# Performance work log

Hardware: AMD Instinct MI355X
Metric: run time of the kernel (lower is better)

Reference implementation:

```python
import jax, jax.numpy as jnp
import numpy as np

ENC_DIM = 1024
NUM_HEADS = 16
HEAD_DIM = ENC_DIM // NUM_HEADS
D_FF = 4 * ENC_DIM
EPS = 1e-5


def _layernorm(x, g, b):
    mu = jnp.mean(x, axis=-1, keepdims=True)
    var = jnp.mean((x - mu) ** 2, axis=-1, keepdims=True)
    return (x - mu) * jax.lax.rsqrt(var + EPS) * g + b


def setup_inputs() -> dict:
    key = jax.random.key(0)
    ks = jax.random.split(key, 12)
    s = 1.0 / np.sqrt(ENC_DIM)
    sf = 1.0 / np.sqrt(D_FF)
    x = jax.random.normal(ks[0], (2, 2048, ENC_DIM), dtype=jnp.float32)
    return {
        "x": x,
        "ln1_g": jnp.ones((ENC_DIM,), jnp.float32),
        "ln1_b": jnp.zeros((ENC_DIM,), jnp.float32),
        "wq": jax.random.uniform(ks[1], (ENC_DIM, ENC_DIM), jnp.float32, -s, s),
        "bq": jax.random.uniform(ks[2], (ENC_DIM,), jnp.float32, -s, s),
        "wk": jax.random.uniform(ks[3], (ENC_DIM, ENC_DIM), jnp.float32, -s, s),
        "bk": jax.random.uniform(ks[4], (ENC_DIM,), jnp.float32, -s, s),
        "wv": jax.random.uniform(ks[5], (ENC_DIM, ENC_DIM), jnp.float32, -s, s),
        "bv": jax.random.uniform(ks[6], (ENC_DIM,), jnp.float32, -s, s),
        "wo": jax.random.uniform(ks[7], (ENC_DIM, ENC_DIM), jnp.float32, -s, s),
        "bo": jax.random.uniform(ks[8], (ENC_DIM,), jnp.float32, -s, s),
        "w1": jax.random.uniform(ks[9], (ENC_DIM, D_FF), jnp.float32, -s, s),
        "b1": jax.random.uniform(ks[10], (D_FF,), jnp.float32, -s, s),
        "w2": jax.random.uniform(ks[11], (D_FF, ENC_DIM), jnp.float32, -sf, sf),
        "b2": jnp.zeros((ENC_DIM,), jnp.float32),
        "ln2_g": jnp.ones((ENC_DIM,), jnp.float32),
        "ln2_b": jnp.zeros((ENC_DIM,), jnp.float32),
    }


def reference(x, ln1_g, ln1_b, wq, bq, wk, bk, wv, bv, wo, bo, w1, b1, w2, b2, ln2_g, ln2_b):
    B, S, D = x.shape
    h = _layernorm(x, ln1_g, ln1_b)
    # QKV projections -> (B, H, S, hd)
    def split_heads(t):
        return t.reshape(B, S, NUM_HEADS, HEAD_DIM).transpose(0, 2, 1, 3)
    q = split_heads(h @ wq + bq)
    k = split_heads(h @ wk + bk)
    v = split_heads(h @ wv + bv)
    scores = jnp.einsum("bhqd,bhkd->bhqk", q, k) / np.sqrt(HEAD_DIM)
    probs = jax.nn.softmax(scores, axis=-1)
    attn = jnp.einsum("bhqk,bhkd->bhqd", probs, v)
    attn = attn.transpose(0, 2, 1, 3).reshape(B, S, D)
    x = attn @ wo + bo + x  # residual 1
    h2 = _layernorm(x, ln2_g, ln2_b)
    mlp = jax.nn.gelu(h2 @ w1 + b1, approximate=False) @ w2 + b2
    return x + mlp
```

## Files before the change

kernel.cpp:

```cpp
#include <hip/hip_runtime.h>

typedef unsigned short u16;
typedef unsigned int u32;
typedef __bf16 bf16x8 __attribute__((ext_vector_type(8)));
typedef float floatx4 __attribute__((ext_vector_type(4)));

__device__ __forceinline__ u16 f2bf(float f) {
    u32 u = __float_as_uint(f);
    u = (u + 0x7FFFu + ((u >> 16) & 1u)) >> 16;
    return (u16)u;
}

__device__ __forceinline__ void gld_lds16(const u16* g, u16* l) {
    __builtin_amdgcn_global_load_lds(
        (const __attribute__((address_space(1))) u32*)g,
        (__attribute__((address_space(3))) u32*)l, 16, 0, 0);
}

__device__ __forceinline__ float gelu_exact(float v) {
    const float z = fabsf(v) * 0.70710678118f;
    const float t = __builtin_amdgcn_rcpf(1.0f + 0.3275911f * z);
    const float e = __builtin_amdgcn_exp2f(-z * z * 1.44269504f);
    float poly = 1.061405429f;
    poly = poly * t - 1.453152027f;
    poly = poly * t + 1.421413741f;
    poly = poly * t - 0.284496736f;
    poly = poly * t + 0.254829592f;
    float erfz = 1.0f - poly * t * e;
    erfz = copysignf(erfz, v);
    return 0.5f * v * (1.0f + erfz);
}

__global__ __launch_bounds__(256) void transpose_cvt4(
    const float* __restrict__ s0, const float* __restrict__ s1,
    const float* __restrict__ s2, const float* __restrict__ s3,
    u16* __restrict__ d0, u16* __restrict__ d1,
    u16* __restrict__ d2, u16* __restrict__ d3)
{
    __shared__ float t[32][33];
    const int z = blockIdx.z;
    const float* src = z == 0 ? s0 : (z == 1 ? s1 : (z == 2 ? s2 : s3));
    u16* dst = z == 0 ? d0 : (z == 1 ? d1 : (z == 2 ? d2 : d3));
    const int bm = blockIdx.x * 32, bk = blockIdx.y * 32;
    const int tx = threadIdx.x & 31, ty = threadIdx.x >> 5;
    #pragma unroll
    for (int i = ty; i < 32; i += 8)
        t[i][tx] = src[(long)(bk + i) * 1024 + bm + tx];
    __syncthreads();
    #pragma unroll
    for (int i = ty; i < 32; i += 8)
        dst[(long)(bm + i) * 1024 + bk + tx] = f2bf(t[tx][i]);
}

__global__ __launch_bounds__(256) void transpose_cvt(
    const float* __restrict__ src, u16* __restrict__ dst, int K, int M)
{
    __shared__ float t[32][33];
    const int bm = blockIdx.x * 32, bk = blockIdx.y * 32;
    const int tx = threadIdx.x & 31, ty = threadIdx.x >> 5;
    #pragma unroll
    for (int i = ty; i < 32; i += 8)
        t[i][tx] = src[(long)(bk + i) * M + bm + tx];
    __syncthreads();
    #pragma unroll
    for (int i = ty; i < 32; i += 8)
        dst[(long)(bm + i) * K + bk + tx] = f2bf(t[tx][i]);
}

__global__ __launch_bounds__(256) void ln_kernel(
    const float* __restrict__ x, const float* __restrict__ g,
    const float* __restrict__ bta, u16* __restrict__ out)
{
    const int row = blockIdx.x;
    const int tid = threadIdx.x;
    const float4 v = ((const float4*)(x + (long)row * 1024))[tid];
    float s  = v.x + v.y + v.z + v.w;
    float s2 = v.x*v.x + v.y*v.y + v.z*v.z + v.w*v.w;
    #pragma unroll
    for (int off = 1; off < 64; off <<= 1) {
        s  += __shfl_xor(s, off);
        s2 += __shfl_xor(s2, off);
    }
    __shared__ float red[8];
    const int wave = tid >> 6, lane = tid & 63;
    if (lane == 0) { red[wave] = s; red[4 + wave] = s2; }
    __syncthreads();
    s  = red[0] + red[1] + red[2] + red[3];
    s2 = red[4] + red[5] + red[6] + red[7];
    const float mu   = s * (1.0f / 1024.0f);
    const float var  = s2 * (1.0f / 1024.0f) - mu * mu;
    const float rstd = rsqrtf(var + 1e-5f);
    const int c = tid << 2;
    ushort4 o;
    o.x = f2bf((v.x - mu) * rstd * g[c + 0] + bta[c + 0]);
    o.y = f2bf((v.y - mu) * rstd * g[c + 1] + bta[c + 1]);
    o.z = f2bf((v.z - mu) * rstd * g[c + 2] + bta[c + 2]);
    o.w = f2bf((v.w - mu) * rstd * g[c + 3] + bta[c + 3]);
    ((ushort4*)(out + (long)row * 1024))[tid] = o;
}

__global__ __launch_bounds__(256) void add_kernel(
    float* __restrict__ out, const float* __restrict__ p1)
{
    const int t = blockIdx.x * 256 + threadIdx.x;
    const float4 a = ((const float4*)out)[t];
    const float4 c = ((const float4*)p1)[t];
    float4 o;
    o.x = a.x + c.x;
    o.y = a.y + c.y;
    o.z = a.z + c.z;
    o.w = a.w + c.w;
    ((float4*)out)[t] = o;
}

__global__ __launch_bounds__(256) void vtrans_kernel(
    const u16* __restrict__ V, u16* __restrict__ Vt)
{
    __shared__ u16 t[64][72];
    const int bh = blockIdx.y, s0 = blockIdx.x << 6;
    const int tid = threadIdx.x;
    const long base = (long)bh * 2048 * 64;
    const int row = tid >> 2, seg = tid & 3;
    *(uint4*)&t[row][seg << 3] =
        *(const uint4*)(V + base + (long)(s0 + row) * 64 + (seg << 3));
    *(uint4*)&t[row][(seg + 4) << 3] =
        *(const uint4*)(V + base + (long)(s0 + row) * 64 + ((seg + 4) << 3));
    __syncthreads();
    #pragma unroll
    for (int half = 0; half < 2; ++half) {
        const int sl = (seg + (half << 2)) << 3;
        u16 tmp[8];
        #pragma unroll
        for (int j = 0; j < 8; ++j) tmp[j] = t[sl + j][row];
        *(uint4*)(Vt + base + (long)row * 2048 + s0 + sl) = *(uint4*)tmp;
    }
}

template<int MODE>
__global__ __launch_bounds__(512, 2) void gemm256_kernel(
    const u16* __restrict__ A, const u16* __restrict__ Bt,
    const float* __restrict__ bias0, const float* __restrict__ bias1,
    const float* __restrict__ bias2, void* __restrict__ outv, int K, int M)
{
    __shared__ u16 As[2][256 * 64];
    __shared__ u16 Bs[2][256 * 64];
    const int tid = threadIdx.x, lane = tid & 63, wave = tid >> 6;
    const int wr = wave >> 2, wc = wave & 3;
    const int lrow = lane & 15, quad = lane >> 4, sl = lrow & 7;

    const int nwg = gridDim.x * gridDim.y;
    const int lin = blockIdx.x + gridDim.x * blockIdx.y;
    const int wg  = (lin & 7) * (nwg >> 3) + (lin >> 3);
    const int bx  = wg % gridDim.x;
    const int by  = wg / gridDim.x;

    const long rowbase = (long)by * 256;
    const long colbase = (long)bx * 256;

    const u16* gA[4]; int lA[4];
    const u16* gB[4]; int lB[4];
    #pragma unroll
    for (int i = 0; i < 4; ++i) {
        const int cid = (i << 9) + tid;
        const int rl = cid >> 3, p = cid & 7, q = p ^ (rl & 7);
        gA[i] = A  + (rowbase + rl) * (long)K + (q << 3);
        gB[i] = Bt + (colbase + rl) * (long)K + (q << 3);
        lA[i] = rl * 64 + (p << 3);
        lB[i] = rl * 64 + (p << 3);
    }

    floatx4 acc[8][4];
    #pragma unroll
    for (int i = 0; i < 8; ++i)
        #pragma unroll
        for (int j = 0; j < 4; ++j)
            acc[i][j] = floatx4{0.f, 0.f, 0.f, 0.f};

    #pragma unroll
    for (int i = 0; i < 4; ++i) { gld_lds16(gA[i], As[0] + lA[i]); gA[i] += 64; }
    #pragma unroll
    for (int i = 0; i < 4; ++i) { gld_lds16(gB[i], Bs[0] + lB[i]); gB[i] += 64; }
    asm volatile("s_waitcnt vmcnt(0)" ::: "memory");
    __builtin_amdgcn_s_barrier();
    __builtin_amdgcn_sched_barrier(0);

    const int niter = K >> 6;
    int cur = 0;
    for (int t = 0; t < niter; ++t) {
        if (t + 1 < niter) {
            #pragma unroll
            for (int i = 0; i < 4; ++i) { gld_lds16(gA[i], As[cur ^ 1] + lA[i]); gA[i] += 64; }
            #pragma unroll
            for (int i = 0; i < 4; ++i) { gld_lds16(gB[i], Bs[cur ^ 1] + lB[i]); gB[i] += 64; }
        }

        const u16* as = As[cur];
        const u16* bs = Bs[cur];

        bf16x8 bfr[4][2];
        #pragma unroll
        for (int ns = 0; ns < 4; ++ns)
            #pragma unroll
            for (int kc = 0; kc < 2; ++kc)
                bfr[ns][kc] = *(const bf16x8*)
                    &bs[((wc << 6) + (ns << 4) + lrow) * 64 + ((((kc << 2) + quad) ^ sl) << 3)];

        #pragma unroll
        for (int p = 0; p < 4; ++p) {
            bf16x8 af[2][2];
            #pragma unroll
            for (int m = 0; m < 2; ++m)
                #pragma unroll
                for (int kc = 0; kc < 2; ++kc)
                    af[m][kc] = *(const bf16x8*)
                        &as[((wr << 7) + ((p * 2 + m) << 4) + lrow) * 64 + ((((kc << 2) + quad) ^ sl) << 3)];
            __builtin_amdgcn_s_setprio(1);
            #pragma unroll
            for (int kc = 0; kc < 2; ++kc)
                #pragma unroll
                for (int m = 0; m < 2; ++m)
                    #pragma unroll
                    for (int ns = 0; ns < 4; ++ns)
                        acc[p * 2 + m][ns] = __builtin_amdgcn_mfma_f32_16x16x32_bf16(
                            af[m][kc], bfr[ns][kc], acc[p * 2 + m][ns], 0, 0, 0);
            __builtin_amdgcn_s_setprio(0);
        }

        asm volatile("s_waitcnt lgkmcnt(0)" ::: "memory");
        asm volatile("s_waitcnt vmcnt(0)" ::: "memory");
        __builtin_amdgcn_s_barrier();
        __builtin_amdgcn_sched_barrier(0);
        cur ^= 1;
    }

    #pragma unroll
    for (int ms = 0; ms < 8; ++ms) {
        #pragma unroll
        for (int ns = 0; ns < 4; ++ns) {
            const long col = colbase + (wc << 6) + (ns << 4) + lrow;
            float bv;
            if constexpr (MODE == 0) {
                const int which = (int)(col >> 10);
                const float* bp = which == 0 ? bias0 : (which == 1 ? bias1 : bias2);
                bv = bp[col & 1023];
            } else {
                bv = bias0[col];
            }
            #pragma unroll
            for (int r = 0; r < 4; ++r) {
                const long row = rowbase + (wr << 7) + (ms << 4) + (quad << 2) + r;
                float v = acc[ms][ns][r] + bv;
                if constexpr (MODE == 0) {
                    const long which = col >> 10;
                    if (which == 0) v *= 0.18033688f;
                    const long b = row >> 11, s = row & 2047;
                    const long h = (col >> 6) & 15, d = col & 63;
                    ((u16*)outv)[which * 4194304 + (((b << 4) + h) * 2048 + s) * 64 + d] = f2bf(v);
                } else {
                    ((u16*)outv)[row * M + col] = f2bf(gelu_exact(v));
                }
            }
        }
    }
}

__global__ __launch_bounds__(512, 2) void gemm_ff2_kernel(
    const u16* __restrict__ A, const u16* __restrict__ Bt,
    const float* __restrict__ bias0, const float* __restrict__ res,
    float* __restrict__ part1, float* __restrict__ out, int K, int M)
{
    __shared__ u16 As[2][128 * 64];
    __shared__ u16 Bs[2][128 * 64];
    const int tid = threadIdx.x, lane = tid & 63, wave = tid >> 6;
    const int wr = wave >> 2, wc = wave & 3;
    const int lrow = lane & 15, quad = lane >> 4, sl = lrow & 7;

    const int nwg = gridDim.x * gridDim.y * gridDim.z;
    const int lin = blockIdx.x + gridDim.x * (blockIdx.y + gridDim.y * blockIdx.z);
    const int wg  = (lin & 7) * (nwg >> 3) + (lin >> 3);
    const int bx  = wg % gridDim.x;
    const int rest = wg / gridDim.x;
    const int by  = rest % gridDim.y;
    const int bz  = rest / gridDim.y;

    const long rowbase = (long)by * 128;
    const long colbase = (long)bx * 128;
    const int kstart = bz * (K >> 1);
    const int kend   = kstart + (K >> 1);

    const u16* gA[2]; int lA[2];
    const u16* gB[2]; int lB[2];
    #pragma unroll
    for (int i = 0; i < 2; ++i) {
        const int cid = (i << 9) + tid;
        const int rl = cid >> 3, p = cid & 7, q = p ^ (rl & 7);
        gA[i] = A  + (rowbase + rl) * (long)K + kstart + (q << 3);
        gB[i] = Bt + (colbase + rl) * (long)K + kstart + (q << 3);
        lA[i] = rl * 64 + (p << 3);
        lB[i] = rl * 64 + (p << 3);
    }

    floatx4 acc[4][2];
    #pragma unroll
    for (int i = 0; i < 4; ++i)
        #pragma unroll
        for (int j = 0; j < 2; ++j)
            acc[i][j] = floatx4{0.f, 0.f, 0.f, 0.f};

    #pragma unroll
    for (int i = 0; i < 2; ++i) { gld_lds16(gA[i], As[0] + lA[i]); gA[i] += 64; }
    #pragma unroll
    for (int i = 0; i < 2; ++i) { gld_lds16(gB[i], Bs[0] + lB[i]); gB[i] += 64; }
    asm volatile("s_waitcnt vmcnt(0)" ::: "memory");
    __builtin_amdgcn_s_barrier();
    __builtin_amdgcn_sched_barrier(0);

    const int niter = (kend - kstart) >> 6;
    int cur = 0;
    for (int t = 0; t < niter; ++t) {
        if (t + 1 < niter) {
            #pragma unroll
            for (int i = 0; i < 2; ++i) { gld_lds16(gA[i], As[cur ^ 1] + lA[i]); gA[i] += 64; }
            #pragma unroll
            for (int i = 0; i < 2; ++i) { gld_lds16(gB[i], Bs[cur ^ 1] + lB[i]); gB[i] += 64; }
        }

        const u16* as = As[cur];
        const u16* bs = Bs[cur];

        bf16x8 bfr[2][2], af[4][2];
        #pragma unroll
        for (int ns = 0; ns < 2; ++ns)
            #pragma unroll
            for (int kc = 0; kc < 2; ++kc)
                bfr[ns][kc] = *(const bf16x8*)
                    &bs[((wc << 5) + (ns << 4) + lrow) * 64 + ((((kc << 2) + quad) ^ sl) << 3)];
        #pragma unroll
        for (int m = 0; m < 4; ++m)
            #pragma unroll
            for (int kc = 0; kc < 2; ++kc)
                af[m][kc] = *(const bf16x8*)
                    &as[((wr << 6) + (m << 4) + lrow) * 64 + ((((kc << 2) + quad) ^ sl) << 3)];

        __builtin_amdgcn_s_setprio(1);
        #pragma unroll
        for (int kc = 0; kc < 2; ++kc)
            #pragma unroll
            for (int m = 0; m < 4; ++m)
                #pragma unroll
                for (int ns = 0; ns < 2; ++ns)
                    acc[m][ns] = __builtin_amdgcn_mfma_f32_16x16x32_bf16(
                        af[m][kc], bfr[ns][kc], acc[m][ns], 0, 0, 0);
        __builtin_amdgcn_s_setprio(0);

        asm volatile("s_waitcnt lgkmcnt(0)" ::: "memory");
        asm volatile("s_waitcnt vmcnt(0)" ::: "memory");
        __builtin_amdgcn_s_barrier();
        __builtin_amdgcn_sched_barrier(0);
        cur ^= 1;
    }

    float* tgt = bz ? part1 : out;
    #pragma unroll
    for (int m = 0; m < 4; ++m) {
        #pragma unroll
        for (int ns = 0; ns < 2; ++ns) {
            const long col = colbase + (wc << 5) + (ns << 4) + lrow;
            #pragma unroll
            for (int r = 0; r < 4; ++r) {
                const long row = rowbase + (wr << 6) + (m << 4) + (quad << 2) + r;
                const long idx = row * M + col;
                float v = acc[m][ns][r];
                if (bz == 0)
                    tgt[idx] = v + bias0[col] + res[idx];
                else
                    tgt[idx] = v;
            }
        }
    }
}

__global__ __launch_bounds__(256) void gemm_oproj_kernel(
    const u16* __restrict__ A, const u16* __restrict__ Bt,
    const float* __restrict__ bias0, const float* __restrict__ res,
    float* __restrict__ out, int K, int M)
{
    constexpr int MS = 2, NIB = 2;
    __shared__ u16 As[128 * 64];
    __shared__ u16 Bs[64 * 64];
    const int tid = threadIdx.x, lane = tid & 63, wave = tid >> 6;
    const int wm = wave << 5, wn = 0;
    const int lrow = lane & 15, quad = lane >> 4;
    const int sl = lrow & 7;

    const int nwg = gridDim.x * gridDim.y;
    const int lin = blockIdx.x + gridDim.x * blockIdx.y;
    const int wg  = (lin & 7) * (nwg >> 3) + (lin >> 3);
    const int bx  = wg % gridDim.x;
    const int by  = wg / gridDim.x;

    const long rowbase = (long)by * 128;
    const long colbase = (long)bx * 64;

    const u16* gA[4]; int lA[4];
    #pragma unroll
    for (int i = 0; i < 4; ++i) {
        const int cid = (i << 6) + lane;
        const int rl = cid >> 3, p = cid & 7, q = p ^ (rl & 7);
        gA[i] = A + (rowbase + (wave << 5) + rl) * (long)K + (q << 3);
        lA[i] = ((wave << 5) + rl) * 64 + (p << 3);
    }
    const u16* gB[NIB]; int lB[NIB];
    #pragma unroll
    for (int i = 0; i < NIB; ++i) {
        const int cid = (i << 6) + lane;
        const int rl = cid >> 3, p = cid & 7, q = p ^ (rl & 7);
        gB[i] = Bt + (colbase + (wave << 4) + rl) * (long)K + (q << 3);
        lB[i] = ((wave << 4) + rl) * 64 + (p << 3);
    }

    floatx4 acc[MS][4];
    #pragma unroll
    for (int i = 0; i < MS; ++i)
        #pragma unroll
        for (int j = 0; j < 4; ++j)
            acc[i][j] = floatx4{0.f, 0.f, 0.f, 0.f};

    for (int k0 = 0; k0 < K; k0 += 64) {
        __syncthreads();
        #pragma unroll
        for (int i = 0; i < 4; ++i) { gld_lds16(gA[i], As + lA[i]); gA[i] += 64; }
        #pragma unroll
        for (int i = 0; i < NIB; ++i) { gld_lds16(gB[i], Bs + lB[i]); gB[i] += 64; }
        __syncthreads();
        #pragma unroll
        for (int kc = 0; kc < 2; ++kc) {
            const int ph = (((kc << 2) + quad) ^ sl) << 3;
            bf16x8 af[MS], bf[4];
            #pragma unroll
            for (int ms = 0; ms < MS; ++ms)
                af[ms] = *(const bf16x8*)&As[(wm + (ms << 4) + lrow) * 64 + ph];
            #pragma unroll
            for (int ns = 0; ns < 4; ++ns)
                bf[ns] = *(const bf16x8*)&Bs[(wn + (ns << 4) + lrow) * 64 + ph];
            #pragma unroll
            for (int ms = 0; ms < MS; ++ms)
                #pragma unroll
                for (int ns = 0; ns < 4; ++ns)
                    acc[ms][ns] = __builtin_amdgcn_mfma_f32_16x16x32_bf16(
                        af[ms], bf[ns], acc[ms][ns], 0, 0, 0);
        }
    }

    #pragma unroll
    for (int ms = 0; ms < MS; ++ms) {
        #pragma unroll
        for (int ns = 0; ns < 4; ++ns) {
            const long col = colbase + wn + (ns << 4) + lrow;
            const float bv = bias0[col];
            #pragma unroll
            for (int r = 0; r < 4; ++r) {
                const long row = rowbase + wm + (ms << 4) + (quad << 2) + r;
                const long idx = row * M + col;
                out[idx] = acc[ms][ns][r] + bv + res[idx];
            }
        }
    }
}

__global__ __launch_bounds__(512) void attn_kernel(
    const u16* __restrict__ Q, const u16* __restrict__ Kp,
    const u16* __restrict__ Vt, u16* __restrict__ O)
{
    __shared__ u16 Ks[2][4096];
    __shared__ u16 Vs[2][4096];
    __shared__ u16 Ps[8][16][72];
    const int tid = threadIdx.x, lane = tid & 63, wave = tid >> 6;
    const int lrow = lane & 15, quad = lane >> 4;

    const int lin = blockIdx.x;
    const int nl  = ((lin & 7) << 6) + (lin >> 3);
    const int bh  = nl >> 4;
    const int qt  = nl & 15;
    const long kvbase = (long)bh * 2048 * 64;
    const int qbase = (qt << 7) + (wave << 4);

    const int srow = lane >> 3;
    const int schunk = (lane & 7) ^ srow;
    const int c = wave & 3;
    const bool isV = wave >= 4;
    const int lofs = c << 10;
    const u16* g0 = isV
        ? (Vt + kvbase + (long)(((c << 4) + srow) * 2048 + (schunk << 3)))
        : (Kp + kvbase + (long)(((c << 4) + srow) * 64   + (schunk << 3)));
    const u16* g1 = g0 + (isV ? 8 * 2048 : 8 * 64);
    const int gstep = isV ? 64 : 4096;
    u16* lb0 = isV ? &Vs[0][lofs] : &Ks[0][lofs];
    u16* lb1 = isV ? &Vs[1][lofs] : &Ks[1][lofs];

    bf16x8 qf[2];
    #pragma unroll
    for (int h = 0; h < 2; ++h)
        qf[h] = *(const bf16x8*)(Q + kvbase +
            (long)(qbase + lrow) * 64 + (quad << 3) + (h << 5));

    int aoff[4][2];
    #pragma unroll
    for (int ns = 0; ns < 4; ++ns)
        #pragma unroll
        for (int h = 0; h < 2; ++h)
            aoff[ns][h] = ((ns << 4) + lrow) * 64 +
                          (((quad + (h << 2)) ^ (lrow & 7)) << 3);

    floatx4 oacc[4];
    #pragma unroll
    for (int ns = 0; ns < 4; ++ns)
        oacc[ns] = floatx4{0.f, 0.f, 0.f, 0.f};
    float lr = 0.f;

    gld_lds16(g0, lb0);
    gld_lds16(g1, lb0 + 512);
    g0 += gstep; g1 += gstep;

    for (int it = 0; it < 32; ++it) {
        const int cur = it & 1;
        __syncthreads();
        if (it < 31) {
            u16* dst = cur ? lb0 : lb1;
            gld_lds16(g0, dst);
            gld_lds16(g1, dst + 512);
            g0 += gstep; g1 += gstep;
        }
        const u16* ks = &Ks[cur][0];
        const u16* vs = &Vs[cur][0];

        floatx4 st[4];
        __builtin_amdgcn_s_setprio(1);
        #pragma unroll
        for (int ns = 0; ns < 4; ++ns) {
            const bf16x8 af0 = *(const bf16x8*)&ks[aoff[ns][0]];
            const bf16x8 af1 = *(const bf16x8*)&ks[aoff[ns][1]];
            floatx4 z = floatx4{0.f, 0.f, 0.f, 0.f};
            st[ns] = __builtin_amdgcn_mfma_f32_16x16x32_bf16(af0, qf[0], z, 0, 0, 0);
            st[ns] = __builtin_amdgcn_mfma_f32_16x16x32_bf16(af1, qf[1], st[ns], 0, 0, 0);
        }
        __builtin_amdgcn_s_setprio(0);

        float rs = 0.f;
        #pragma unroll
        for (int ns = 0; ns < 4; ++ns) {
            const float p0 = __builtin_amdgcn_exp2f(st[ns][0]);
            const float p1 = __builtin_amdgcn_exp2f(st[ns][1]);
            const float p2 = __builtin_amdgcn_exp2f(st[ns][2]);
            const float p3 = __builtin_amdgcn_exp2f(st[ns][3]);
            rs += (p0 + p1) + (p2 + p3);
            uint2 w;
            w.x = __builtin_amdgcn_perm(__float_as_uint(p1) + 0x8000u,
                                        __float_as_uint(p0) + 0x8000u, 0x07060302u);
            w.y = __builtin_amdgcn_perm(__float_as_uint(p3) + 0x8000u,
                                        __float_as_uint(p2) + 0x8000u, 0x07060302u);
            *(uint2*)&Ps[wave][lrow][(ns << 4) + (quad << 2)] = w;
        }
        rs += __shfl_xor(rs, 16);
        rs += __shfl_xor(rs, 32);
        lr += rs;
        const bf16x8 pf0 = *(const bf16x8*)&Ps[wave][lrow][quad << 3];
        const bf16x8 pf1 = *(const bf16x8*)&Ps[wave][lrow][(quad << 3) + 32];

        __builtin_amdgcn_s_setprio(1);
        #pragma unroll
        for (int ns = 0; ns < 4; ++ns) {
            const bf16x8 vf0 = *(const bf16x8*)&vs[aoff[ns][0]];
            const bf16x8 vf1 = *(const bf16x8*)&vs[aoff[ns][1]];
            oacc[ns] = __builtin_amdgcn_mfma_f32_16x16x32_bf16(pf0, vf0, oacc[ns], 0, 0, 0);
            oacc[ns] = __builtin_amdgcn_mfma_f32_16x16x32_bf16(pf1, vf1, oacc[ns], 0, 0, 0);
        }
        __builtin_amdgcn_s_setprio(0);
    }

    const int b = bh >> 4, h = bh & 15;
    float linv[4];
    #pragma unroll
    for (int r = 0; r < 4; ++r)
        linv[r] = 1.0f / __shfl(lr, (quad << 2) + r);
    #pragma unroll
    for (int ns = 0; ns < 4; ++ns)
        #pragma unroll
        for (int r = 0; r < 4; ++r) {
            const int q = qbase + (quad << 2) + r;
            const long token = (long)b * 2048 + q;
            O[token * 1024 + (h << 6) + (ns << 4) + lrow] =
                f2bf(oacc[ns][r] * linv[r]);
        }
}

extern "C" void kernel_launch(void* const* d_in, const int* in_sizes, int n_in,
                              void* d_out, int out_size, void* d_ws, size_t ws_size,
                              hipStream_t stream)
{
    const float* x     = (const float*)d_in[0];
    const float* ln1_g = (const float*)d_in[1];
    const float* ln1_b = (const float*)d_in[2];
    const float* wq    = (const float*)d_in[3];
    const float* bq    = (const float*)d_in[4];
    const float* wk    = (const float*)d_in[5];
    const float* bk    = (const float*)d_in[6];
    const float* wv    = (const float*)d_in[7];
    const float* bv    = (const float*)d_in[8];
    const float* wo    = (const float*)d_in[9];
    const float* bo    = (const float*)d_in[10];
    const float* w1    = (const float*)d_in[11];
    const float* b1    = (const float*)d_in[12];
    const float* w2    = (const float*)d_in[13];
    const float* b2    = (const float*)d_in[14];
    const float* ln2_g = (const float*)d_in[15];
    const float* ln2_b = (const float*)d_in[16];
    float* out = (float*)d_out;

    char* w = (char*)d_ws;
    const size_t MB = 1024 * 1024;
    u16*   wqkvt = (u16*)(w + 0);
    u16*   wot   = (u16*)(w + 6  * MB);
    u16*   w1t   = (u16*)(w + 8  * MB);
    u16*   w2t   = (u16*)(w + 16 * MB);
    u16*   h1    = (u16*)(w + 24 * MB);
    u16*   qkvb  = (u16*)(w + 32 * MB);
    u16*   vtb   = (u16*)(w + 56 * MB);
    float* x1    = (float*)(w + 64 * MB);
    float* part1 = (float*)(w + 80 * MB);
    u16*   ffb   = (u16*)(w + 32 * MB);
    u16*   qb = qkvb;
    u16*   kb = qkvb + 4194304;
    u16*   vb = qkvb + 8388608;

    transpose_cvt4<<<dim3(32, 32, 4), 256, 0, stream>>>(
        wq, wk, wv, wo, wqkvt, wqkvt + 1048576, wqkvt + 2097152, wot);
    transpose_cvt<<<dim3(128, 32), 256, 0, stream>>>(w1, w1t, 1024, 4096);
    transpose_cvt<<<dim3(32, 128), 256, 0, stream>>>(w2, w2t, 4096, 1024);

    ln_kernel<<<4096, 256, 0, stream>>>(x, ln1_g, ln1_b, h1);

    gemm256_kernel<0><<<dim3(12, 16), 512, 0, stream>>>(
        h1, wqkvt, bq, bk, bv, qkvb, 1024, 3072);

    vtrans_kernel<<<dim3(32, 32), 256, 0, stream>>>(vb, vtb);

    attn_kernel<<<dim3(512), 512, 0, stream>>>(qb, kb, vtb, h1);

    gemm_oproj_kernel<<<dim3(16, 32), 256, 0, stream>>>(
        h1, wot, bo, x, x1, 1024, 1024);

    ln_kernel<<<4096, 256, 0, stream>>>(x1, ln2_g, ln2_b, h1);

    gemm256_kernel<2><<<dim3(16, 16), 512, 0, stream>>>(
        h1, w1t, b1, nullptr, nullptr, ffb, 1024, 4096);

    gemm_ff2_kernel<<<dim3(8, 32, 2), 512, 0, stream>>>(
        ffb, w2t, b2, x1, part1, out, 4096, 1024);

    add_kernel<<<4096, 256, 0, stream>>>(out, part1);
}
```

Before: 345.5 us.

## Split attention over two KV halves and combine partials in separate kernel

```diff
diff --git a/kernel.cpp b/kernel.cpp
--- a/kernel.cpp
+++ b/kernel.cpp
@@ -470,7 +470,8 @@
 
 __global__ __launch_bounds__(512) void attn_kernel(
     const u16* __restrict__ Q, const u16* __restrict__ Kp,
-    const u16* __restrict__ Vt, u16* __restrict__ O)
+    const u16* __restrict__ Vt, float* __restrict__ PO,
+    float* __restrict__ LP)
 {
     __shared__ u16 Ks[2][4096];
     __shared__ u16 Vs[2][4096];
@@ -479,9 +480,10 @@
     const int lrow = lane & 15, quad = lane >> 4;
 
     const int lin = blockIdx.x;
-    const int nl  = ((lin & 7) << 6) + (lin >> 3);
-    const int bh  = nl >> 4;
-    const int qt  = nl & 15;
+    const int nl  = ((lin & 7) << 7) + (lin >> 3);
+    const int bh  = nl >> 5;
+    const int qt  = (nl >> 1) & 15;
+    const int kz  = nl & 1;
     const long kvbase = (long)bh * 2048 * 64;
     const int qbase = (qt << 7) + (wave << 4);
 
@@ -491,8 +493,8 @@
     const bool isV = wave >= 4;
     const int lofs = c << 10;
     const u16* g0 = isV
-        ? (Vt + kvbase + (long)(((c << 4) + srow) * 2048 + (schunk << 3)))
-        : (Kp + kvbase + (long)(((c << 4) + srow) * 64   + (schunk << 3)));
+        ? (Vt + kvbase + (long)(((c << 4) + srow) * 2048 + (kz << 10) + (schunk << 3)))
+        : (Kp + kvbase + (long)(kz << 16) + (long)(((c << 4) + srow) * 64 + (schunk << 3)));
     const u16* g1 = g0 + (isV ? 8 * 2048 : 8 * 64);
     const int gstep = isV ? 64 : 4096;
     u16* lb0 = isV ? &Vs[0][lofs] : &Ks[0][lofs];
@@ -522,10 +524,10 @@
     gld_lds16(g1, lb0 + 512);
     g0 += gstep; g1 += gstep;
 
-    for (int it = 0; it < 32; ++it) {
+    for (int it = 0; it < 16; ++it) {
         const int cur = it & 1;
         __syncthreads();
-        if (it < 31) {
+        if (it < 15) {
             u16* dst = cur ? lb0 : lb1;
             gld_lds16(g0, dst);
             gld_lds16(g1, dst + 512);
@@ -578,20 +580,36 @@
         __builtin_amdgcn_s_setprio(0);
     }
 
-    const int b = bh >> 4, h = bh & 15;
-    float linv[4];
-    #pragma unroll
-    for (int r = 0; r < 4; ++r)
-        linv[r] = 1.0f / __shfl(lr, (quad << 2) + r);
+    float* po = PO + (long)kz * 4194304 + (long)bh * 2048 * 64;
     #pragma unroll
     for (int ns = 0; ns < 4; ++ns)
         #pragma unroll
         for (int r = 0; r < 4; ++r) {
             const int q = qbase + (quad << 2) + r;
-            const long token = (long)b * 2048 + q;
-            O[token * 1024 + (h << 6) + (ns << 4) + lrow] =
-                f2bf(oacc[ns][r] * linv[r]);
-        }
+            po[(long)q * 64 + (ns << 4) + lrow] = oacc[ns][r];
+        }
+    if (quad == 0)
+        LP[kz * 65536 + bh * 2048 + qbase + lrow] = lr;
+}
+
+__global__ __launch_bounds__(256) void attn_combine_kernel(
+    const float* __restrict__ PO, const float* __restrict__ LP,
+    u16* __restrict__ O)
+{
+    const int tid = threadIdx.x;
+    const int row = blockIdx.x * 16 + (tid >> 4);
+    const int d4  = (tid & 15) << 2;
+    const float4 a = *(const float4*)(PO + (long)row * 64 + d4);
+    const float4 b = *(const float4*)(PO + 4194304 + (long)row * 64 + d4);
+    const float rinv = 1.0f / (LP[row] + LP[65536 + row]);
+    const int bh = row >> 11, q = row & 2047;
+    const int bb = bh >> 4, h = bh & 15;
+    ushort4 o;
+    o.x = f2bf((a.x + b.x) * rinv);
+    o.y = f2bf((a.y + b.y) * rinv);
+    o.z = f2bf((a.z + b.z) * rinv);
+    o.w = f2bf((a.w + b.w) * rinv);
+    *(ushort4*)(O + ((long)(bb * 2048 + q) * 1024 + (h << 6) + d4)) = o;
 }
 
 extern "C" void kernel_launch(void* const* d_in, const int* in_sizes, int n_in,
@@ -628,6 +646,8 @@
     u16*   vtb   = (u16*)(w + 56 * MB);
     float* x1    = (float*)(w + 64 * MB);
     float* part1 = (float*)(w + 80 * MB);
+    float* po    = (float*)(w + 64 * MB);
+    float* lp    = (float*)(w + 96 * MB);
     u16*   ffb   = (u16*)(w + 32 * MB);
     u16*   qb = qkvb;
     u16*   kb = qkvb + 4194304;
@@ -645,7 +665,8 @@
 
     vtrans_kernel<<<dim3(32, 32), 256, 0, stream>>>(vb, vtb);
 
-    attn_kernel<<<dim3(512), 512, 0, stream>>>(qb, kb, vtb, h1);
+    attn_kernel<<<dim3(1024), 512, 0, stream>>>(qb, kb, vtb, po, lp);
+    attn_combine_kernel<<<dim3(4096), 256, 0, stream>>>(po, lp, h1);
 
     gemm_oproj_kernel<<<dim3(16, 32), 256, 0, stream>>>(
         h1, wot, bo, x, x1, 1024, 1024);
```

Measured after the change: 371.0 us. 1.07x slower.
